# Optimization experiments

Hardware: AMD Instinct MI355X
Metric: run time of the kernel (lower is better)

The kernel has to match this reference:

```python
import jax, jax.numpy as jnp
import numpy as np

HIDDEN = 1024
N_HEADS = 16
HEAD_DIM = HIDDEN // N_HEADS


def apply_rope(x, freqs):
    # x: [b, s, h, d]; freqs: [s, d//2]
    b, s, h, d = x.shape
    x2 = x.reshape(b, s, h, d // 2, 2)
    x_real, x_imag = x2[..., 0], x2[..., 1]
    cos = jnp.cos(freqs)[None, :, None, :]  # [1, s, 1, d//2]
    sin = jnp.sin(freqs)[None, :, None, :]
    out_real = x_real * cos - x_imag * sin
    out_imag = x_real * sin + x_imag * cos
    return jnp.stack([out_real, out_imag], axis=-1).reshape(b, s, h, d)


def setup_inputs() -> dict:
    key = jax.random.key(0)
    k_x, k_f, k_wq, k_bq, k_wo, k_bo = jax.random.split(key, 6)
    b, s = 2, 2048
    x = jax.random.normal(k_x, (b, s, HIDDEN), dtype=jnp.float32)
    freqs = jax.random.normal(k_f, (s, HEAD_DIM // 2), dtype=jnp.float32)
    lim = 1.0 / np.sqrt(HIDDEN)
    W_qkv = jax.random.uniform(k_wq, (HIDDEN, 3 * HIDDEN), jnp.float32, -lim, lim)
    b_qkv = jax.random.uniform(k_bq, (3 * HIDDEN,), jnp.float32, -lim, lim)
    W_out = jax.random.uniform(k_wo, (HIDDEN, HIDDEN), jnp.float32, -lim, lim)
    b_out = jax.random.uniform(k_bo, (HIDDEN,), jnp.float32, -lim, lim)
    return {"x": x, "freqs": freqs, "W_qkv": W_qkv, "b_qkv": b_qkv,
            "W_out": W_out, "b_out": b_out}


def reference(x, freqs, W_qkv, b_qkv, W_out, b_out):
    b, s, c = x.shape
    h, d = N_HEADS, HEAD_DIM
    qkv = jnp.einsum('bsc,cf->bsf', x, W_qkv) + b_qkv  # [b, s, 3*c]
    qkv = qkv.reshape(b, s, 3, h, d)
    q, k, v = qkv[:, :, 0], qkv[:, :, 1], qkv[:, :, 2]  # [b, s, h, d]
    q = apply_rope(q, freqs)
    k = apply_rope(k, freqs)
    scale = 1.0 / np.sqrt(d).astype(np.float32)
    scores = jnp.einsum('bqhd,bkhd->bhqk', q, k) * scale  # [b, h, s, s]
    attn = jax.nn.softmax(scores, axis=-1)
    out = jnp.einsum('bhqk,bkhd->bqhd', attn, v).reshape(b, s, c)
    return jnp.einsum('bsc,cf->bsf', out, W_out) + b_out
```

## Files before the change

### kernel.cpp

```cpp
#include <hip/hip_runtime.h>
#include <math.h>

constexpr int kB = 2;
constexpr int kS = 2048;
constexpr int kC = 1024;
constexpr int kH = 16;
constexpr int kD = 64;
constexpr int kF = 3072;
constexpr int kT = kB * kS;

typedef __attribute__((ext_vector_type(8))) short short8v;
typedef __attribute__((ext_vector_type(4))) short short4v;
typedef __attribute__((ext_vector_type(4))) float f32x4;
typedef __attribute__((ext_vector_type(16))) float f32x16;

__device__ __forceinline__ short f2bf(float f) {
    unsigned u = __builtin_bit_cast(unsigned, f);
    u += 0x7fffu + ((u >> 16) & 1u);
    return (short)(u >> 16);
}

__device__ __forceinline__ unsigned cvtpk(float a, float b) {
    unsigned r;
    asm("v_cvt_pk_bf16_f32 %0, %1, %2" : "=v"(r) : "v"(a), "v"(b));
    return r;
}

__device__ __forceinline__ unsigned pk_bf16(float a, float b) {
    unsigned ua = __builtin_bit_cast(unsigned, a);
    ua += 0x7fffu + ((ua >> 16) & 1u);
    unsigned ub = __builtin_bit_cast(unsigned, b);
    ub += 0x7fffu + ((ub >> 16) & 1u);
    return (ua >> 16) | (ub & 0xffff0000u);
}

__device__ __forceinline__ void gl_lds16(const void* g, void* l) {
    __builtin_amdgcn_global_load_lds(
        (const __attribute__((address_space(1))) char*)g,
        (__attribute__((address_space(3))) char*)l, 16, 0, 0);
}

__device__ __forceinline__ f32x4 mfma16(short8v a, short8v b, f32x4 c) {
    return __builtin_amdgcn_mfma_f32_16x16x32_bf16(a, b, c, 0, 0, 0);
}
__device__ __forceinline__ f32x16 mfma32(short8v a, short8v b, f32x16 c) {
    return __builtin_amdgcn_mfma_f32_32x32x16_bf16(a, b, c, 0, 0, 0);
}

__device__ __forceinline__ void tcvt_body(const float* __restrict__ w,
                                          short* __restrict__ wt, int K, int N,
                                          int bx, int by, int t, float Ts[64][65]) {
    const int n0 = bx * 64, k0 = by * 64;
    const int r = t >> 4, c4 = (t & 15) * 4;
#pragma unroll
    for (int rr = 0; rr < 64; rr += 16) {
        float4 v = *reinterpret_cast<const float4*>(&w[(size_t)(k0 + r + rr) * N + n0 + c4]);
        Ts[r + rr][c4 + 0] = v.x; Ts[r + rr][c4 + 1] = v.y;
        Ts[r + rr][c4 + 2] = v.z; Ts[r + rr][c4 + 3] = v.w;
    }
    __syncthreads();
#pragma unroll
    for (int rr = 0; rr < 64; rr += 16) {
        int n = r + rr;
        short4v o = { f2bf(Ts[c4 + 0][n]), f2bf(Ts[c4 + 1][n]),
                      f2bf(Ts[c4 + 2][n]), f2bf(Ts[c4 + 3][n]) };
        *reinterpret_cast<short4v*>(&wt[(size_t)(n0 + n) * K + k0 + c4]) = o;
    }
}

__global__ __launch_bounds__(256) void prep_kernel(
    const float* __restrict__ x, short* __restrict__ xb,
    const float* __restrict__ wq, short* __restrict__ wqt,
    const float* __restrict__ wo, short* __restrict__ wot,
    const float* __restrict__ freqs, float* __restrict__ cost,
    float* __restrict__ sint) {
    __shared__ float Ts[64][65];
    const int bid = blockIdx.x, t = threadIdx.x;
    if (bid < 4096) {
        int i = bid * 256 + t;
        float4 v = reinterpret_cast<const float4*>(x)[i];
        short4v o = { f2bf(v.x), f2bf(v.y), f2bf(v.z), f2bf(v.w) };
        reinterpret_cast<short4v*>(xb)[i] = o;
    } else if (bid < 4864) {
        int i = bid - 4096;
        tcvt_body(wq, wqt, kC, kF, i % 48, i / 48, t, Ts);
    } else if (bid < 5120) {
        int i = bid - 4864;
        tcvt_body(wo, wot, kC, kC, i % 16, i / 16, t, Ts);
    } else {
        int i = (bid - 5120) * 256 + t;
        float f = freqs[i];
        float s, c;
        sincosf(f, &s, &c);
        cost[i] = c; sint[i] = s;
    }
}

__device__ __forceinline__ void gemm_main(const short* __restrict__ A,
                                          const short* __restrict__ Bt,
                                          int m0, int n0, short* Als, short* Bls,
                                          f32x4 acc[4][4]) {
    const int tid = threadIdx.x, wid = tid >> 6, lane = tid & 63;
    const int srow = lane >> 3, schunk = lane & 7;
    const int fr = lane & 15, fg = lane >> 4;
    const int wm = (wid >> 1) * 64, wn = (wid & 1) * 64;
    for (int kt = 0; kt < 1024; kt += 64) {
        __syncthreads();
#pragma unroll
        for (int j = 0; j < 4; ++j) {
            int i = wid * 4 + j;
            int row = i * 8 + srow;
            gl_lds16(&A[(size_t)(m0 + row) * 1024 + kt + ((schunk ^ (row & 7)) << 3)],
                     &Als[i * 512]);
        }
#pragma unroll
        for (int j = 0; j < 4; ++j) {
            int i = wid * 4 + j;
            int row = i * 8 + srow;
            gl_lds16(&Bt[(size_t)(n0 + row) * 1024 + kt + ((schunk ^ (row & 7)) << 3)],
                     &Bls[i * 512]);
        }
        __syncthreads();
#pragma unroll
        for (int kk = 0; kk < 2; ++kk) {
            short8v af[4], bf[4];
#pragma unroll
            for (int fm = 0; fm < 4; ++fm) {
                int row = wm + fm * 16 + fr;
                af[fm] = *reinterpret_cast<const short8v*>(
                    &Als[row * 64 + (((fg + 4 * kk) ^ (row & 7)) << 3)]);
            }
#pragma unroll
            for (int fn = 0; fn < 4; ++fn) {
                int row = wn + fn * 16 + fr;
                bf[fn] = *reinterpret_cast<const short8v*>(
                    &Bls[row * 64 + (((fg + 4 * kk) ^ (row & 7)) << 3)]);
            }
#pragma unroll
            for (int fm = 0; fm < 4; ++fm)
#pragma unroll
                for (int fn = 0; fn < 4; ++fn)
                    acc[fm][fn] = mfma16(af[fm], bf[fn], acc[fm][fn]);
        }
    }
}

__global__ __launch_bounds__(256) void qkv_gemm_kernel(
    const short* __restrict__ xb, const short* __restrict__ wqt,
    const float* __restrict__ bias, const float* __restrict__ cost,
    const float* __restrict__ sint,
    short* __restrict__ qg, short* __restrict__ kg, short* __restrict__ vt) {
    __shared__ __attribute__((aligned(16))) short Als[128 * 64];
    __shared__ __attribute__((aligned(16))) short Bls[128 * 64];
    f32x4 acc[4][4] = {};
    const int tid = threadIdx.x, wid = tid >> 6, lane = tid & 63;
    const int m0 = blockIdx.y * 128, n0 = blockIdx.x * 128;
    gemm_main(xb, wqt, m0, n0, Als, Bls, acc);

    const int fr = lane & 15, fg = lane >> 4;
    const int wm = (wid >> 1) * 64, wn = (wid & 1) * 64;
    const int which = (n0 + wn) >> 10;
    const int bidx = m0 >> 11;
#pragma unroll
    for (int fn = 0; fn < 4; ++fn) {
        int col = n0 + wn + fn * 16 + fr;
        float bv = bias[col];
        int d = col & 63;
        int h = (col >> 6) & 15;
        int p0 = d >> 1;
        int odd = d & 1;
#pragma unroll
        for (int fm = 0; fm < 4; ++fm) {
            int r0 = m0 + wm + fm * 16 + fg * 4;
            int s0 = r0 & 2047;
            float c[4];
#pragma unroll
            for (int r = 0; r < 4; ++r) c[r] = acc[fm][fn][r] + bv;
            if (which < 2) {
#pragma unroll
                for (int r = 0; r < 4; ++r) {
                    float cs = cost[(s0 + r) * 32 + p0];
                    float sn = sint[(s0 + r) * 32 + p0];
                    float p = __shfl_xor(c[r], 1);
                    float o = odd ? fmaf(p, sn, c[r] * cs) : fmaf(-p, sn, c[r] * cs);
                    c[r] = (which == 0) ? o * 0.1803368801f : o;
                }
                short* dst = which ? kg : qg;
                size_t base = ((size_t)(bidx * 16 + h) * 2048 + s0) * 64 + d;
#pragma unroll
                for (int r = 0; r < 4; ++r) dst[base + (size_t)r * 64] = f2bf(c[r]);
            } else {
                short4v o = { f2bf(c[0]), f2bf(c[1]), f2bf(c[2]), f2bf(c[3]) };
                *reinterpret_cast<short4v*>(
                    &vt[((size_t)(bidx * 16 + h) * 64 + d) * 2048 + s0]) = o;
            }
        }
    }
}

__global__ __launch_bounds__(256, 4) void attn_mfma_kernel(
    const short* __restrict__ qg, const short* __restrict__ kg,
    const short* __restrict__ vt, short* __restrict__ ab) {
    __shared__ __attribute__((aligned(16))) short LDSBUF[16384];
    const int tid = threadIdx.x, wid = tid >> 6, lane = tid & 63;
    const int l31 = lane & 31, hi = lane >> 5;
    const int p = wid >> 1;
    const int wq = wid & 1;
    const int r8 = lane >> 3, c8 = lane & 7;
    const int soff = 8 * (c8 ^ r8);

    const int bid = blockIdx.x;
    const int swz = (bid & 7) * 128 + (bid >> 3);
    const int bh = swz >> 5;
    const int q0 = (swz & 31) * 64 + wq * 32;

    const short* qb = qg + (size_t)bh * 2048 * 64;
    const short* kb = kg + (size_t)bh * 2048 * 64;
    const short* vb = vt + (size_t)bh * 64 * 2048;

    short8v qf[4];
#pragma unroll
    for (int kkq = 0; kkq < 4; ++kkq)
        qf[kkq] = *reinterpret_cast<const short8v*>(
            &qb[(size_t)(q0 + l31) * 64 + kkq * 16 + hi * 8]);

    f32x16 o[2] = {};
    float l_i = 0.f;

    auto stage = [&](int t, int buf) {
        const int kt = t * 32;
        short* Kd = LDSBUF + buf * 8192 + p * 2048 + (wq * 8) * 64;
        const short* Ks = kb + (size_t)(p * 1024 + kt) * 64;
#pragma unroll
        for (int j = 0; j < 2; ++j) {
            int row = j * 16 + wq * 8 + r8;
            gl_lds16(Ks + (size_t)row * 64 + soff, Kd + j * 1024);
        }
        short* Vd = LDSBUF + buf * 8192 + 4096 + (wid * 8) * 64;
        const int s = c8 ^ r8;
#pragma unroll
        for (int j = 0; j < 2; ++j) {
            int d = j * 32 + wid * 8 + r8;
            gl_lds16(vb + (size_t)d * 2048 + (s >> 2) * 1024 + kt + (s & 3) * 8,
                     Vd + j * 2048);
        }
    };

    stage(0, 0);
    __syncthreads();

    short8v pb_prev[2];
    for (int t = 0; t <= 32; ++t) {
        const int cur = t & 1, prv = cur ^ 1;
        short8v kf[4], vf0[2], vf1[2];
        if (t < 32) {
            const short* Kb = LDSBUF + cur * 8192 + p * 2048;
#pragma unroll
            for (int kkq = 0; kkq < 4; ++kkq)
                kf[kkq] = *reinterpret_cast<const short8v*>(
                    &Kb[l31 * 64 + (((kkq * 2 + hi) ^ (l31 & 7)) << 3)]);
        }
        if (t > 0) {
            const short* Vb = LDSBUF + prv * 8192 + 4096;
#pragma unroll
            for (int kk = 0; kk < 2; ++kk) {
                vf0[kk] = *reinterpret_cast<const short8v*>(
                    &Vb[l31 * 64 + (((p * 4 + kk * 2 + hi) ^ (l31 & 7)) << 3)]);
                vf1[kk] = *reinterpret_cast<const short8v*>(
                    &Vb[(32 + l31) * 64 + (((p * 4 + kk * 2 + hi) ^ (l31 & 7)) << 3)]);
            }
        }
        __syncthreads();
        if (t + 1 < 32) stage(t + 1, prv);

        f32x16 sacc = {};
        if (t < 32) {
#pragma unroll
            for (int kkq = 0; kkq < 4; ++kkq)
                sacc = mfma32(kf[kkq], qf[kkq], sacc);
        }
        if (t > 0) {
#pragma unroll
            for (int kk = 0; kk < 2; ++kk) {
                o[0] = mfma32(vf0[kk], pb_prev[kk], o[0]);
                o[1] = mfma32(vf1[kk], pb_prev[kk], o[1]);
            }
        }
        if (t < 32) {
#pragma unroll
            for (int r = 0; r < 16; ++r) sacc[r] = __builtin_amdgcn_exp2f(sacc[r]);
            unsigned c[8];
#pragma unroll
            for (int i = 0; i < 8; ++i) c[i] = cvtpk(sacc[2 * i], sacc[2 * i + 1]);
#pragma unroll
            for (int kk = 0; kk < 2; ++kk) {
                unsigned a0 = c[kk * 4 + 0], a1 = c[kk * 4 + 1];
                unsigned a2 = c[kk * 4 + 2], a3 = c[kk * 4 + 3];
                unsigned s0x = (unsigned)__shfl_xor((int)a0, 32);
                unsigned s1x = (unsigned)__shfl_xor((int)a1, 32);
                unsigned s2x = (unsigned)__shfl_xor((int)a2, 32);
                unsigned s3x = (unsigned)__shfl_xor((int)a3, 32);
                uint4 w;
                w.x = hi ? s2x : a0;
                w.y = hi ? s3x : a1;
                w.z = hi ? a2 : s0x;
                w.w = hi ? a3 : s1x;
                pb_prev[kk] = __builtin_bit_cast(short8v, w);
            }
            float t8[8];
#pragma unroll
            for (int r = 0; r < 8; ++r) t8[r] = sacc[r] + sacc[r + 8];
            float t4[4];
#pragma unroll
            for (int r = 0; r < 4; ++r) t4[r] = t8[r] + t8[r + 4];
            float rs = (t4[0] + t4[1]) + (t4[2] + t4[3]);
            rs += __shfl_xor(rs, 32);
            l_i += rs;
        }
        __syncthreads();
    }

    float* olds = reinterpret_cast<float*>(LDSBUF + 4096);
    float* lls  = olds + 2 * 2304;
    if (p == 1) {
        float* ob = olds + wq * 2304 + lane * 36;
#pragma unroll
        for (int i = 0; i < 4; ++i) {
            f32x4 w0 = { o[0][4 * i + 0], o[0][4 * i + 1], o[0][4 * i + 2], o[0][4 * i + 3] };
            *reinterpret_cast<f32x4*>(ob + i * 4) = w0;
            f32x4 w1 = { o[1][4 * i + 0], o[1][4 * i + 1], o[1][4 * i + 2], o[1][4 * i + 3] };
            *reinterpret_cast<f32x4*>(ob + 16 + i * 4) = w1;
        }
        lls[wq * 64 + lane] = l_i;
    }
    __syncthreads();
    if (p == 0) {
        float* ob = olds + wq * 2304 + lane * 36;
#pragma unroll
        for (int i = 0; i < 4; ++i) {
            f32x4 w0 = *reinterpret_cast<const f32x4*>(ob + i * 4);
            f32x4 w1 = *reinterpret_cast<const f32x4*>(ob + 16 + i * 4);
#pragma unroll
            for (int j = 0; j < 4; ++j) {
                o[0][4 * i + j] += w0[j];
                o[1][4 * i + j] += w1[j];
            }
        }
        l_i += lls[wq * 64 + lane];

        const float inv = 1.f / l_i;
        short* ep = LDSBUF + wid * 2048;
        const int q = l31;
#pragma unroll
        for (int fd = 0; fd < 2; ++fd)
#pragma unroll
            for (int i = 0; i < 4; ++i) {
                int d0 = fd * 32 + 8 * i + 4 * hi;
                uint2 w;
                w.x = pk_bf16(o[fd][4 * i + 0] * inv, o[fd][4 * i + 1] * inv);
                w.y = pk_bf16(o[fd][4 * i + 2] * inv, o[fd][4 * i + 3] * inv);
                *reinterpret_cast<uint2*>(&ep[q * 64 + (d0 ^ (8 * (q & 3)))]) = w;
            }
        __builtin_amdgcn_s_waitcnt(0);
        const int bb = bh >> 4, hh = bh & 15;
        const int wrow = r8, wcol = c8;
#pragma unroll
        for (int j = 0; j < 4; ++j) {
            int row = j * 8 + wrow;
            short8v tv = *reinterpret_cast<const short8v*>(
                &ep[row * 64 + ((8 * wcol) ^ (8 * (row & 3)))]);
            int s = q0 + row;
            *reinterpret_cast<short8v*>(
                &ab[(size_t)(bb * 2048 + s) * 1024 + hh * 64 + 8 * wcol]) = tv;
        }
    }
}

__global__ __launch_bounds__(256) void out_gemm_kernel(
    const short* __restrict__ ab, const short* __restrict__ wot,
    const float* __restrict__ bias, float* __restrict__ out) {
    __shared__ __attribute__((aligned(16))) short Als[128 * 64];
    __shared__ __attribute__((aligned(16))) short Bls[128 * 64];
    f32x4 acc[4][4] = {};
    const int tid = threadIdx.x, wid = tid >> 6, lane = tid & 63;
    const int m0 = blockIdx.y * 128, n0 = blockIdx.x * 128;
    gemm_main(ab, wot, m0, n0, Als, Bls, acc);
    const int fr = lane & 15, fg = lane >> 4;
    const int wm = (wid >> 1) * 64, wn = (wid & 1) * 64;
#pragma unroll
    for (int fn = 0; fn < 4; ++fn) {
        int col = n0 + wn + fn * 16 + fr;
        float bv = bias[col];
#pragma unroll
        for (int fm = 0; fm < 4; ++fm) {
            int r0 = m0 + wm + fm * 16 + fg * 4;
#pragma unroll
            for (int r = 0; r < 4; ++r)
                out[(size_t)(r0 + r) * 1024 + col] = acc[fm][fn][r] + bv;
        }
    }
}

extern "C" void kernel_launch(void* const* d_in, const int* in_sizes, int n_in,
                              void* d_out, int out_size, void* d_ws, size_t ws_size,
                              hipStream_t stream) {
    const float* x     = (const float*)d_in[0];
    const float* freqs = (const float*)d_in[1];
    const float* W_qkv = (const float*)d_in[2];
    const float* b_qkv = (const float*)d_in[3];
    const float* W_out = (const float*)d_in[4];
    const float* b_out = (const float*)d_in[5];
    float* out = (float*)d_out;

    char* w = (char*)d_ws;
    short* xb  = (short*)w;  w += (size_t)kT * kC * 2;
    short* wqt = (short*)w;  w += (size_t)kF * kC * 2;
    short* wot = (short*)w;  w += (size_t)kC * kC * 2;
    short* qgw = (short*)w;  w += (size_t)kB * kH * kS * kD * 2;
    short* kgw = (short*)w;  w += (size_t)kB * kH * kS * kD * 2;
    short* vtw = (short*)w;  w += (size_t)kB * kH * kS * kD * 2;
    short* abw = (short*)w;  w += (size_t)kT * kC * 2;
    float* costt = (float*)w; w += (size_t)kS * (kD / 2) * 4;
    float* sintt = (float*)w; w += (size_t)kS * (kD / 2) * 4;

    prep_kernel<<<dim3(5376), 256, 0, stream>>>(x, xb, W_qkv, wqt, W_out, wot,
                                                freqs, costt, sintt);
    qkv_gemm_kernel<<<dim3(kF / 128, kT / 128), 256, 0, stream>>>(
        xb, wqt, b_qkv, costt, sintt, qgw, kgw, vtw);
    attn_mfma_kernel<<<dim3(1024), 256, 0, stream>>>(qgw, kgw, vtw, abw);
    out_gemm_kernel<<<dim3(kC / 128, kT / 128), 256, 0, stream>>>(abw, wot, b_out, out);
}
```

Before: 133.3 us.

## Simplify attention loop pipeline and shrink output GEMM tile to 128x64

After: 126.1 us. 1.06x faster.

```diff
diff --git a/kernel.cpp b/kernel.cpp
--- a/kernel.cpp
+++ b/kernel.cpp
@@ -249,73 +249,60 @@
     stage(0, 0);
     __syncthreads();
 
-    short8v pb_prev[2];
-    for (int t = 0; t <= 32; ++t) {
-        const int cur = t & 1, prv = cur ^ 1;
-        short8v kf[4], vf0[2], vf1[2];
-        if (t < 32) {
-            const short* Kb = LDSBUF + cur * 8192 + p * 2048;
-#pragma unroll
-            for (int kkq = 0; kkq < 4; ++kkq)
-                kf[kkq] = *reinterpret_cast<const short8v*>(
-                    &Kb[l31 * 64 + (((kkq * 2 + hi) ^ (l31 & 7)) << 3)]);
-        }
-        if (t > 0) {
-            const short* Vb = LDSBUF + prv * 8192 + 4096;
-#pragma unroll
-            for (int kk = 0; kk < 2; ++kk) {
-                vf0[kk] = *reinterpret_cast<const short8v*>(
-                    &Vb[l31 * 64 + (((p * 4 + kk * 2 + hi) ^ (l31 & 7)) << 3)]);
-                vf1[kk] = *reinterpret_cast<const short8v*>(
-                    &Vb[(32 + l31) * 64 + (((p * 4 + kk * 2 + hi) ^ (l31 & 7)) << 3)]);
-            }
-        }
-        __syncthreads();
-        if (t + 1 < 32) stage(t + 1, prv);
+    for (int t = 0; t < 32; ++t) {
+        const int buf = t & 1;
+        if (t + 1 < 32) stage(t + 1, buf ^ 1);
+        const short* Kb = LDSBUF + buf * 8192 + p * 2048;
+        const short* Vb = LDSBUF + buf * 8192 + 4096;
 
         f32x16 sacc = {};
-        if (t < 32) {
-#pragma unroll
-            for (int kkq = 0; kkq < 4; ++kkq)
-                sacc = mfma32(kf[kkq], qf[kkq], sacc);
-        }
-        if (t > 0) {
-#pragma unroll
-            for (int kk = 0; kk < 2; ++kk) {
-                o[0] = mfma32(vf0[kk], pb_prev[kk], o[0]);
-                o[1] = mfma32(vf1[kk], pb_prev[kk], o[1]);
-            }
-        }
-        if (t < 32) {
-#pragma unroll
-            for (int r = 0; r < 16; ++r) sacc[r] = __builtin_amdgcn_exp2f(sacc[r]);
-            unsigned c[8];
-#pragma unroll
-            for (int i = 0; i < 8; ++i) c[i] = cvtpk(sacc[2 * i], sacc[2 * i + 1]);
-#pragma unroll
-            for (int kk = 0; kk < 2; ++kk) {
-                unsigned a0 = c[kk * 4 + 0], a1 = c[kk * 4 + 1];
-                unsigned a2 = c[kk * 4 + 2], a3 = c[kk * 4 + 3];
-                unsigned s0x = (unsigned)__shfl_xor((int)a0, 32);
-                unsigned s1x = (unsigned)__shfl_xor((int)a1, 32);
-                unsigned s2x = (unsigned)__shfl_xor((int)a2, 32);
-                unsigned s3x = (unsigned)__shfl_xor((int)a3, 32);
-                uint4 w;
-                w.x = hi ? s2x : a0;
-                w.y = hi ? s3x : a1;
-                w.z = hi ? a2 : s0x;
-                w.w = hi ? a3 : s1x;
-                pb_prev[kk] = __builtin_bit_cast(short8v, w);
-            }
-            float t8[8];
-#pragma unroll
-            for (int r = 0; r < 8; ++r) t8[r] = sacc[r] + sacc[r + 8];
-            float t4[4];
-#pragma unroll
-            for (int r = 0; r < 4; ++r) t4[r] = t8[r] + t8[r + 4];
-            float rs = (t4[0] + t4[1]) + (t4[2] + t4[3]);
-            rs += __shfl_xor(rs, 32);
-            l_i += rs;
+#pragma unroll
+        for (int kkq = 0; kkq < 4; ++kkq) {
+            short8v a = *reinterpret_cast<const short8v*>(
+                &Kb[l31 * 64 + (((kkq * 2 + hi) ^ (l31 & 7)) << 3)]);
+            sacc = mfma32(a, qf[kkq], sacc);
+        }
+
+#pragma unroll
+        for (int r = 0; r < 16; ++r) sacc[r] = __builtin_amdgcn_exp2f(sacc[r]);
+        float t8[8];
+#pragma unroll
+        for (int r = 0; r < 8; ++r) t8[r] = sacc[r] + sacc[r + 8];
+        float t4[4];
+#pragma unroll
+        for (int r = 0; r < 4; ++r) t4[r] = t8[r] + t8[r + 4];
+        float rs = (t4[0] + t4[1]) + (t4[2] + t4[3]);
+        rs += __shfl_xor(rs, 32);
+        l_i += rs;
+
+        unsigned c[8];
+#pragma unroll
+        for (int i = 0; i < 8; ++i) c[i] = cvtpk(sacc[2 * i], sacc[2 * i + 1]);
+        short8v pb[2];
+#pragma unroll
+        for (int kk = 0; kk < 2; ++kk) {
+            unsigned a0 = c[kk * 4 + 0], a1 = c[kk * 4 + 1];
+            unsigned a2 = c[kk * 4 + 2], a3 = c[kk * 4 + 3];
+            unsigned s0x = (unsigned)__shfl_xor((int)a0, 32);
+            unsigned s1x = (unsigned)__shfl_xor((int)a1, 32);
+            unsigned s2x = (unsigned)__shfl_xor((int)a2, 32);
+            unsigned s3x = (unsigned)__shfl_xor((int)a3, 32);
+            uint4 w;
+            w.x = hi ? s2x : a0;
+            w.y = hi ? s3x : a1;
+            w.z = hi ? a2 : s0x;
+            w.w = hi ? a3 : s1x;
+            pb[kk] = __builtin_bit_cast(short8v, w);
+        }
+
+#pragma unroll
+        for (int kk = 0; kk < 2; ++kk) {
+            short8v v0 = *reinterpret_cast<const short8v*>(
+                &Vb[l31 * 64 + (((p * 4 + kk * 2 + hi) ^ (l31 & 7)) << 3)]);
+            short8v v1 = *reinterpret_cast<const short8v*>(
+                &Vb[(32 + l31) * 64 + (((p * 4 + kk * 2 + hi) ^ (l31 & 7)) << 3)]);
+            o[0] = mfma32(v0, pb[kk], o[0]);
+            o[1] = mfma32(v1, pb[kk], o[1]);
         }
         __syncthreads();
     }
@@ -380,15 +367,55 @@
     const short* __restrict__ ab, const short* __restrict__ wot,
     const float* __restrict__ bias, float* __restrict__ out) {
     __shared__ __attribute__((aligned(16))) short Als[128 * 64];
-    __shared__ __attribute__((aligned(16))) short Bls[128 * 64];
-    f32x4 acc[4][4] = {};
+    __shared__ __attribute__((aligned(16))) short Bls[64 * 64];
+    f32x4 acc[4][2] = {};
     const int tid = threadIdx.x, wid = tid >> 6, lane = tid & 63;
-    const int m0 = blockIdx.y * 128, n0 = blockIdx.x * 128;
-    gemm_main(ab, wot, m0, n0, Als, Bls, acc);
+    const int srow = lane >> 3, schunk = lane & 7;
     const int fr = lane & 15, fg = lane >> 4;
-    const int wm = (wid >> 1) * 64, wn = (wid & 1) * 64;
-#pragma unroll
-    for (int fn = 0; fn < 4; ++fn) {
+    const int wm = (wid >> 1) * 64, wn = (wid & 1) * 32;
+    const int m0 = blockIdx.y * 128, n0 = blockIdx.x * 64;
+
+    for (int kt = 0; kt < 1024; kt += 64) {
+        __syncthreads();
+#pragma unroll
+        for (int j = 0; j < 4; ++j) {
+            int i = wid * 4 + j;
+            int row = i * 8 + srow;
+            gl_lds16(&ab[(size_t)(m0 + row) * 1024 + kt + ((schunk ^ (row & 7)) << 3)],
+                     &Als[i * 512]);
+        }
+#pragma unroll
+        for (int j = 0; j < 2; ++j) {
+            int i = wid * 2 + j;
+            int row = i * 8 + srow;
+            gl_lds16(&wot[(size_t)(n0 + row) * 1024 + kt + ((schunk ^ (row & 7)) << 3)],
+                     &Bls[i * 512]);
+        }
+        __syncthreads();
+#pragma unroll
+        for (int kk = 0; kk < 2; ++kk) {
+            short8v af[4], bf[2];
+#pragma unroll
+            for (int fm = 0; fm < 4; ++fm) {
+                int row = wm + fm * 16 + fr;
+                af[fm] = *reinterpret_cast<const short8v*>(
+                    &Als[row * 64 + (((fg + 4 * kk) ^ (row & 7)) << 3)]);
+            }
+#pragma unroll
+            for (int fn = 0; fn < 2; ++fn) {
+                int row = wn + fn * 16 + fr;
+                bf[fn] = *reinterpret_cast<const short8v*>(
+                    &Bls[row * 64 + (((fg + 4 * kk) ^ (row & 7)) << 3)]);
+            }
+#pragma unroll
+            for (int fm = 0; fm < 4; ++fm)
+#pragma unroll
+                for (int fn = 0; fn < 2; ++fn)
+                    acc[fm][fn] = mfma16(af[fm], bf[fn], acc[fm][fn]);
+        }
+    }
+#pragma unroll
+    for (int fn = 0; fn < 2; ++fn) {
         int col = n0 + wn + fn * 16 + fr;
         float bv = bias[col];
 #pragma unroll
@@ -428,5 +455,5 @@
     qkv_gemm_kernel<<<dim3(kF / 128, kT / 128), 256, 0, stream>>>(
         xb, wqt, b_qkv, costt, sintt, qgw, kgw, vtw);
     attn_mfma_kernel<<<dim3(1024), 256, 0, stream>>>(qgw, kgw, vtw, abw);
-    out_gemm_kernel<<<dim3(kC / 128, kT / 128), 256, 0, stream>>>(abw, wot, b_out, out);
-}
+    out_gemm_kernel<<<dim3(kC / 64, kT / 128), 256, 0, stream>>>(abw, wot, b_out, out);
+}
```
